# Kernel tuning notes

Measured on AMD Instinct MI355X. Metric: run time of the kernel, lower is better.

The kernel has to match this reference:

```python
import jax, jax.numpy as jnp
import numpy as np

EPS = 1e-5  # torch LayerNorm default


def _ln(x, w, b):
    m = jnp.mean(x, axis=-1, keepdims=True)
    v = jnp.mean((x - m) ** 2, axis=-1, keepdims=True)
    return (x - m) / jnp.sqrt(v + EPS) * w + b


def _conv1x1(x, w, b):
    # x: [B,C,H,W], w: [O,C], b: [O]
    return jnp.einsum('bchw,oc->bohw', x, w) + b[None, :, None, None]


def setup_inputs() -> dict:
    key = jax.random.key(0)
    ks = jax.random.split(key, 5)
    B, Cin, H, W = 8, 384, 64, 64
    D, N = 128, 512
    s = lambda k, shape, scale=0.02: jax.random.normal(k, shape, jnp.float32) * scale
    return {
        'x': jax.random.normal(ks[0], (B, Cin, H, W), jnp.float32),
        'DR': jax.random.normal(ks[1], (N, D), jnp.float32),
        'conv_in_w': s(ks[2], (D, Cin)),
        'conv_in_b': jnp.zeros((D,), jnp.float32),
        'sem_w': s(ks[3], (D, D)),
        'sem_b': jnp.zeros((D,), jnp.float32),
        'norm1_w': jnp.ones((D,), jnp.float32),
        'norm1_b': jnp.zeros((D,), jnp.float32),
        'norm2_w': jnp.ones((D,), jnp.float32),
        'norm2_b': jnp.zeros((D,), jnp.float32),
        'conv_out_w': s(ks[4], (Cin, D)),
        'conv_out_b': jnp.zeros((Cin,), jnp.float32),
    }


def reference(x, DR, conv_in_w, conv_in_b, sem_w, sem_b, norm1_w, norm1_b,
              norm2_w, norm2_b, conv_out_w, conv_out_b):
    B, _, H, W = x.shape
    N = DR.shape[0]
    x_align = _conv1x1(x, conv_in_w, conv_in_b)                      # [B,D,H,W]
    x_sem = _conv1x1(x_align, sem_w, sem_b)                          # semantic_extra (1x1 conv)
    x_sem = x_sem.transpose(0, 2, 3, 1).reshape(B, H * W, -1)        # [B,HW,D]
    x_sem = _ln(x_sem, norm1_w, norm1_b)
    dr = _ln(DR, norm2_w, norm2_b).T                                 # [D,N] (same for all batches)
    # NOTE: original applies norm_1 TWICE for the numerator (faithful quirk)
    c_u = jnp.einsum('bld,dn->bln', _ln(x_sem, norm1_w, norm1_b), dr)  # [B,HW,N]
    c_d_l = jnp.sqrt(jnp.sum(x_sem ** 2, axis=-1, keepdims=True))      # [B,HW,1]
    c_d_r = jnp.sqrt(jnp.sum(dr ** 2, axis=0, keepdims=True))[None]    # [1,1,N]
    sim = c_u / (c_d_l * c_d_r)
    sim_soft = jax.nn.softmax(sim, axis=-1)                          # [B,HW,N]
    sim2d = sim_soft.transpose(0, 2, 1).reshape(B, N, H, W)
    degrad = jnp.einsum('bln,dn->bdl', sim_soft, dr).reshape(B, -1, H, W)  # [B,D,H,W]
    # pow-mask with per-batch min-max normalization
    mask_v = jnp.max(sim2d ** 3, axis=1, keepdims=True)              # [B,1,H,W]
    mn = jnp.min(mask_v.reshape(B, -1), axis=1).reshape(B, 1, 1, 1)
    mx = jnp.max(mask_v.reshape(B, -1), axis=1).reshape(B, 1, 1, 1)
    mask_v = 1.0 - (mask_v - mn) / (mx - mn)
    # topk row selection (torch fancy indexing gives [B,B,K,N]; squeeze(1) is a no-op for B>1)
    max_values = jnp.max(sim_soft, axis=2)                           # [B,HW]
    K = (H * W) // 50
    _, top_idx = jax.lax.top_k(max_values, K)                        # [B,K]
    results = jnp.take(sim_soft, top_idx, axis=1)                    # [B,B,K,N]
    out_img = _conv1x1(degrad, conv_out_w, conv_out_b)               # [B,Cin,H,W]
    return (mask_v, out_img, results)
```

## Files before the change

### kernel.cpp

```cpp
#include <hip/hip_runtime.h>
#include <cstdint>

#define EPS 1e-5f
#define BB   8
#define CIN  384
#define HWs  4096
#define LT   32768
#define DD   128
#define NN   512
#define TOPK 81

typedef short short8 __attribute__((ext_vector_type(8)));
typedef float f32x4  __attribute__((ext_vector_type(4)));

__device__ __forceinline__ unsigned short f2bf(float x) {
  unsigned u = __float_as_uint(x);
  u += 0x7fffu + ((u >> 16) & 1u);
  return (unsigned short)(u >> 16);
}
__device__ __forceinline__ float bf2f(unsigned u16) {
  return __uint_as_float(u16 << 16);
}
__device__ __forceinline__ void put_frag(unsigned short* buf, int tile, int rc, int k, float v) {
  int ks = k >> 5, g = (k >> 3) & 3, j = k & 7;
  int basehw = ((tile * 4 + ks) * 2) * 512 + (g * 16 + rc) * 8 + j;
  unsigned short hi = f2bf(v);
  buf[basehw] = hi;
  buf[basehw + 512] = f2bf(v - bf2f(hi));
}

__global__ __launch_bounds__(64) void k_dr(const float* __restrict__ DR,
    const float* __restrict__ w2, const float* __restrict__ b2,
    const float* __restrict__ w1, const float* __restrict__ b1,
    unsigned short* __restrict__ drwF, unsigned short* __restrict__ drlnF,
    float* __restrict__ t2, float* __restrict__ rcr) {
  int n = blockIdx.x;
  int lane = threadIdx.x;
  const float* row = DR + n * DD;
  float x0 = row[lane], x1 = row[lane + 64];
  float s = x0 + x1, sq = x0 * x0 + x1 * x1;
  #pragma unroll
  for (int o = 32; o; o >>= 1) { s += __shfl_xor(s, o); sq += __shfl_xor(sq, o); }
  float m = s * (1.f / 128.f);
  float v = sq * (1.f / 128.f) - m * m;
  float inv = rsqrtf(v + EPS);
  float y0 = (x0 - m) * inv * w2[lane] + b2[lane];
  float y1 = (x1 - m) * inv * w2[lane + 64] + b2[lane + 64];
  int nt = n >> 4, cc = n & 15;
  put_frag(drwF, nt, cc, lane, y0 * w1[lane]);
  put_frag(drwF, nt, cc, lane + 64, y1 * w1[lane + 64]);
  int ks = n >> 5, gB = (n >> 3) & 3, j = n & 7;
  {
    int d = lane;
    unsigned short hi = f2bf(y0);
    int base = (((d >> 4) * 16 + ks) * 2) * 512 + (gB * 16 + (d & 15)) * 8 + j;
    drlnF[base] = hi;
    drlnF[base + 512] = f2bf(y0 - bf2f(hi));
  }
  {
    int d = lane + 64;
    unsigned short hi = f2bf(y1);
    int base = (((d >> 4) * 16 + ks) * 2) * 512 + (gB * 16 + (d & 15)) * 8 + j;
    drlnF[base] = hi;
    drlnF[base + 512] = f2bf(y1 - bf2f(hi));
  }
  float pt2 = y0 * b1[lane] + y1 * b1[lane + 64];
  float pss = y0 * y0 + y1 * y1;
  #pragma unroll
  for (int o = 32; o; o >>= 1) { pt2 += __shfl_xor(pt2, o); pss += __shfl_xor(pss, o); }
  if (lane == 0) { t2[n] = pt2; rcr[n] = rsqrtf(pss); }
}

__global__ __launch_bounds__(256) void k_bprep(const float* __restrict__ src,
                                               unsigned short* __restrict__ dst,
                                               int K) {
  int rt = blockIdx.x, kb = blockIdx.y;
  int t = threadIdx.x, m = t >> 4, kg = t & 15;
  int k0 = kb * 128 + kg * 8;
  const float* s = src + (size_t)(rt * 16 + m) * K + k0;
  float4 f0 = *(const float4*)s;
  float4 f1 = *(const float4*)(s + 4);
  float vs[8] = {f0.x, f0.y, f0.z, f0.w, f1.x, f1.y, f1.z, f1.w};
  short8 hi, lo;
  #pragma unroll
  for (int j = 0; j < 8; ++j) {
    unsigned short h = f2bf(vs[j]);
    hi[j] = (short)h;
    lo[j] = (short)f2bf(vs[j] - bf2f(h));
  }
  int nkt = K >> 5;
  int ks = k0 >> 5, g = (k0 >> 3) & 3;
  short8* D8 = (short8*)dst;
  int base = ((rt * nkt + ks) * 2) * 64 + g * 16 + m;
  D8[base] = hi;
  D8[base + 64] = lo;
}

__global__ __launch_bounds__(256, 3) void k_convsem(const float* __restrict__ x,
    const unsigned short* __restrict__ WinF, const float* __restrict__ bin,
    const unsigned short* __restrict__ semWF, const float* __restrict__ sb,
    const float* __restrict__ w1, const float* __restrict__ b1,
    unsigned short* __restrict__ ApF, float* __restrict__ rclv) {
  __shared__ float xt[CIN * 33];
  __shared__ float sredS[32][4], sredQ[32][4];
  __shared__ float rowM[32], rowI[32];
  int t = threadIdx.x;
  int w = t >> 6, lane = t & 63, m = lane & 15, g = lane >> 4;
  int l0 = blockIdx.x * 32;
  int b = l0 >> 12, hw0 = l0 & 4095;
  {
    const float* xs = x + (size_t)b * CIN * HWs + (size_t)(t >> 3) * HWs + hw0 + (t & 7) * 4;
    float4 v[12];
    #pragma unroll
    for (int r = 0; r < 12; ++r)
      v[r] = *(const float4*)(xs + (size_t)(r * 32) * HWs);
    #pragma unroll
    for (int r = 0; r < 12; ++r) {
      float* d = &xt[(r * 32 + (t >> 3)) * 33 + (t & 7) * 4];
      d[0] = v[r].x; d[1] = v[r].y; d[2] = v[r].z; d[3] = v[r].w;
    }
  }
  __syncthreads();
  const short8* B8 = (const short8*)WinF;
  f32x4 acc[2][2];
  #pragma unroll
  for (int lt = 0; lt < 2; ++lt)
    #pragma unroll
    for (int j2 = 0; j2 < 2; ++j2) acc[lt][j2] = (f32x4){0.f, 0.f, 0.f, 0.f};
  for (int ks = 0; ks < 12; ++ks) {
    short8 ah[2], al[2];
    #pragma unroll
    for (int lt = 0; lt < 2; ++lt) {
      #pragma unroll
      for (int j = 0; j < 8; ++j) {
        float xv = xt[(ks * 32 + g * 8 + j) * 33 + lt * 16 + m];
        unsigned short h = f2bf(xv);
        ah[lt][j] = (short)h;
        al[lt][j] = (short)f2bf(xv - bf2f(h));
      }
    }
    #pragma unroll
    for (int j2 = 0; j2 < 2; ++j2) {
      int dt = w * 2 + j2;
      short8 bh = B8[((dt * 12 + ks) * 2 + 0) * 64 + lane];
      short8 bl = B8[((dt * 12 + ks) * 2 + 1) * 64 + lane];
      #pragma unroll
      for (int lt = 0; lt < 2; ++lt) {
        acc[lt][j2] = __builtin_amdgcn_mfma_f32_16x16x32_bf16(ah[lt], bh, acc[lt][j2], 0, 0, 0);
        acc[lt][j2] = __builtin_amdgcn_mfma_f32_16x16x32_bf16(ah[lt], bl, acc[lt][j2], 0, 0, 0);
        acc[lt][j2] = __builtin_amdgcn_mfma_f32_16x16x32_bf16(al[lt], bh, acc[lt][j2], 0, 0, 0);
      }
    }
  }
  __syncthreads();
  unsigned int* plane = (unsigned int*)xt;
  {
    float bia[2] = {bin[w * 32 + m], bin[w * 32 + 16 + m]};
    #pragma unroll
    for (int lt = 0; lt < 2; ++lt)
      #pragma unroll
      for (int j2 = 0; j2 < 2; ++j2)
        #pragma unroll
        for (int r = 0; r < 4; ++r) {
          float v = acc[lt][j2][r] + bia[j2];
          unsigned short h = f2bf(v);
          unsigned short lo = f2bf(v - bf2f(h));
          plane[(lt * 16 + g * 4 + r) * 132 + (w * 2 + j2) * 16 + m] =
              (unsigned)h | ((unsigned)lo << 16);
        }
  }
  __syncthreads();
  const short8* S8 = (const short8*)semWF;
  f32x4 acc2[2][2];
  #pragma unroll
  for (int lt = 0; lt < 2; ++lt)
    #pragma unroll
    for (int j2 = 0; j2 < 2; ++j2) acc2[lt][j2] = (f32x4){0.f, 0.f, 0.f, 0.f};
  #pragma unroll
  for (int ks2 = 0; ks2 < 4; ++ks2) {
    short8 ah2[2], al2[2];
    #pragma unroll
    for (int lt = 0; lt < 2; ++lt) {
      const unsigned* src = &plane[(lt * 16 + m) * 132 + ks2 * 32 + g * 8];
      uint4 p0 = *(const uint4*)(src);
      uint4 p1 = *(const uint4*)(src + 4);
      unsigned uu[8] = {p0.x, p0.y, p0.z, p0.w, p1.x, p1.y, p1.z, p1.w};
      unsigned* ahp = (unsigned*)&ah2[lt];
      unsigned* alp = (unsigned*)&al2[lt];
      #pragma unroll
      for (int jj = 0; jj < 4; ++jj) {
        unsigned e0 = uu[2 * jj], e1 = uu[2 * jj + 1];
        ahp[jj] = (e0 & 0xffffu) | (e1 << 16);
        alp[jj] = (e0 >> 16) | (e1 & 0xffff0000u);
      }
    }
    #pragma unroll
    for (int j2 = 0; j2 < 2; ++j2) {
      int dt = w * 2 + j2;
      short8 bh = S8[((dt * 4 + ks2) * 2 + 0) * 64 + lane];
      short8 bl = S8[((dt * 4 + ks2) * 2 + 1) * 64 + lane];
      #pragma unroll
      for (int lt = 0; lt < 2; ++lt) {
        acc2[lt][j2] = __builtin_amdgcn_mfma_f32_16x16x32_bf16(ah2[lt], bh, acc2[lt][j2], 0, 0, 0);
        acc2[lt][j2] = __builtin_amdgcn_mfma_f32_16x16x32_bf16(ah2[lt], bl, acc2[lt][j2], 0, 0, 0);
        acc2[lt][j2] = __builtin_amdgcn_mfma_f32_16x16x32_bf16(al2[lt], bh, acc2[lt][j2], 0, 0, 0);
      }
    }
  }
  {
    float bia2[2] = {sb[w * 32 + m], sb[w * 32 + 16 + m]};
    #pragma unroll
    for (int lt = 0; lt < 2; ++lt)
      #pragma unroll
      for (int j2 = 0; j2 < 2; ++j2)
        #pragma unroll
        for (int r = 0; r < 4; ++r) acc2[lt][j2][r] += bia2[j2];
  }
  float s1[2][4], q1[2][4];
  #pragma unroll
  for (int lt = 0; lt < 2; ++lt)
    #pragma unroll
    for (int r = 0; r < 4; ++r) {
      float a = acc2[lt][0][r], b2v = acc2[lt][1][r];
      s1[lt][r] = a + b2v;
      q1[lt][r] = a * a + b2v * b2v;
    }
  #pragma unroll
  for (int o = 1; o < 16; o <<= 1)
    #pragma unroll
    for (int lt = 0; lt < 2; ++lt)
      #pragma unroll
      for (int r = 0; r < 4; ++r) {
        s1[lt][r] += __shfl_xor(s1[lt][r], o);
        q1[lt][r] += __shfl_xor(q1[lt][r], o);
      }
  if (m == 0) {
    #pragma unroll
    for (int lt = 0; lt < 2; ++lt)
      #pragma unroll
      for (int r = 0; r < 4; ++r) {
        sredS[lt * 16 + g * 4 + r][w] = s1[lt][r];
        sredQ[lt * 16 + g * 4 + r][w] = q1[lt][r];
      }
  }
  __syncthreads();
  if (t < 32) {
    float S = sredS[t][0] + sredS[t][1] + sredS[t][2] + sredS[t][3];
    float Q = sredQ[t][0] + sredQ[t][1] + sredQ[t][2] + sredQ[t][3];
    float mu = S * (1.f / 128.f);
    float var = Q * (1.f / 128.f) - mu * mu;
    rowM[t] = mu;
    rowI[t] = rsqrtf(var + EPS);
  }
  __syncthreads();
  float w1v[2] = {w1[w * 32 + m], w1[w * 32 + 16 + m]};
  float b1v[2] = {b1[w * 32 + m], b1[w * 32 + 16 + m]};
  #pragma unroll
  for (int lt = 0; lt < 2; ++lt)
    #pragma unroll
    for (int r = 0; r < 4; ++r) {
      float mu = rowM[lt * 16 + g * 4 + r];
      float iv = rowI[lt * 16 + g * 4 + r];
      float y0 = (acc2[lt][0][r] - mu) * iv * w1v[0] + b1v[0];
      float y1 = (acc2[lt][1][r] - mu) * iv * w1v[1] + b1v[1];
      acc2[lt][0][r] = y0; acc2[lt][1][r] = y1;
      s1[lt][r] = y0 + y1;
      q1[lt][r] = y0 * y0 + y1 * y1;
    }
  #pragma unroll
  for (int o = 1; o < 16; o <<= 1)
    #pragma unroll
    for (int lt = 0; lt < 2; ++lt)
      #pragma unroll
      for (int r = 0; r < 4; ++r) {
        s1[lt][r] += __shfl_xor(s1[lt][r], o);
        q1[lt][r] += __shfl_xor(q1[lt][r], o);
      }
  if (m == 0) {
    #pragma unroll
    for (int lt = 0; lt < 2; ++lt)
      #pragma unroll
      for (int r = 0; r < 4; ++r) {
        sredS[lt * 16 + g * 4 + r][w] = s1[lt][r];
        sredQ[lt * 16 + g * 4 + r][w] = q1[lt][r];
      }
  }
  __syncthreads();
  if (t < 32) {
    float S = sredS[t][0] + sredS[t][1] + sredS[t][2] + sredS[t][3];
    float Q = sredQ[t][0] + sredQ[t][1] + sredQ[t][2] + sredQ[t][3];
    float m2 = S * (1.f / 128.f);
    float v2 = Q * (1.f / 128.f) - m2 * m2;
    float inv2 = rsqrtf(v2 + EPS);
    float rcl = rsqrtf(Q);
    rowM[t] = m2;
    rowI[t] = inv2 * rcl;
    rclv[l0 + t] = rcl;
  }
  __syncthreads();
  float* planef = (float*)xt;
  #pragma unroll
  for (int lt = 0; lt < 2; ++lt)
    #pragma unroll
    for (int r = 0; r < 4; ++r) {
      float m2 = rowM[lt * 16 + g * 4 + r];
      float sc = rowI[lt * 16 + g * 4 + r];
      planef[(lt * 16 + g * 4 + r) * 132 + w * 32 + m] = (acc2[lt][0][r] - m2) * sc;
      planef[(lt * 16 + g * 4 + r) * 132 + w * 32 + 16 + m] = (acc2[lt][1][r] - m2) * sc;
    }
  __syncthreads();
  short8* O8 = (short8*)ApF;
  #pragma unroll
  for (int it = 0; it < 2; ++it) {
    int idx = it * 256 + t;
    int l = idx & 31, dq = idx >> 5;
    const float* src = &planef[l * 132 + dq * 8];
    float4 f0 = *(const float4*)src;
    float4 f1 = *(const float4*)(src + 4);
    float vs[8] = {f0.x, f0.y, f0.z, f0.w, f1.x, f1.y, f1.z, f1.w};
    short8 hi, lo;
    #pragma unroll
    for (int j = 0; j < 8; ++j) {
      unsigned short h = f2bf(vs[j]);
      hi[j] = (short)h;
      lo[j] = (short)f2bf(vs[j] - bf2f(h));
    }
    int ltg = (l0 + l) >> 4;
    int idx8 = ((ltg * 4 + (dq >> 2)) * 2) * 64 + (dq & 3) * 16 + (l & 15);
    O8[idx8] = hi;
    O8[idx8 + 64] = lo;
  }
}

__global__ __launch_bounds__(256) void k_scores(const unsigned short* __restrict__ ApF,
    const unsigned short* __restrict__ drwF, const float* __restrict__ t2g,
    const float* __restrict__ rcrg, const float* __restrict__ rclg,
    unsigned short* __restrict__ pF, float* __restrict__ maxv) {
  __shared__ __align__(16) float sredM[32][4];
  __shared__ __align__(16) float sredS[32][4];
  __shared__ __align__(16) unsigned short plds[32 * 520];
  int t = threadIdx.x;
  int w = t >> 6, lane = t & 63, c = lane & 15, g = lane >> 4;
  int l0 = blockIdx.x * 32;
  int lt0 = blockIdx.x * 2;
  const short8* A8 = (const short8*)ApF;
  const short8* B8 = (const short8*)drwF;
  f32x4 acc[2][8];
  #pragma unroll
  for (int il = 0; il < 2; ++il)
    #pragma unroll
    for (int jn = 0; jn < 8; ++jn) acc[il][jn] = (f32x4){0.f, 0.f, 0.f, 0.f};
  #pragma unroll
  for (int ks = 0; ks < 4; ++ks) {
    short8 ah0 = A8[((lt0 * 4 + ks) * 2 + 0) * 64 + lane];
    short8 al0 = A8[((lt0 * 4 + ks) * 2 + 1) * 64 + lane];
    short8 ah1 = A8[(((lt0 + 1) * 4 + ks) * 2 + 0) * 64 + lane];
    short8 al1 = A8[(((lt0 + 1) * 4 + ks) * 2 + 1) * 64 + lane];
    #pragma unroll
    for (int jn = 0; jn < 8; ++jn) {
      int nt = w * 8 + jn;
      short8 bh = B8[((nt * 4 + ks) * 2 + 0) * 64 + lane];
      short8 bl = B8[((nt * 4 + ks) * 2 + 1) * 64 + lane];
      acc[0][jn] = __builtin_amdgcn_mfma_f32_16x16x32_bf16(ah0, bh, acc[0][jn], 0, 0, 0);
      acc[0][jn] = __builtin_amdgcn_mfma_f32_16x16x32_bf16(ah0, bl, acc[0][jn], 0, 0, 0);
      acc[0][jn] = __builtin_amdgcn_mfma_f32_16x16x32_bf16(al0, bh, acc[0][jn], 0, 0, 0);
      acc[1][jn] = __builtin_amdgcn_mfma_f32_16x16x32_bf16(ah1, bh, acc[1][jn], 0, 0, 0);
      acc[1][jn] = __builtin_amdgcn_mfma_f32_16x16x32_bf16(ah1, bl, acc[1][jn], 0, 0, 0);
      acc[1][jn] = __builtin_amdgcn_mfma_f32_16x16x32_bf16(al1, bh, acc[1][jn], 0, 0, 0);
    }
  }
  float rcrv[8], t2v[8];
  #pragma unroll
  for (int jn = 0; jn < 8; ++jn) {
    int n = w * 128 + jn * 16 + c;
    rcrv[jn] = rcrg[n]; t2v[jn] = t2g[n];
  }
  float rclr[2][4];
  #pragma unroll
  for (int il = 0; il < 2; ++il)
    #pragma unroll
    for (int r = 0; r < 4; ++r)
      rclr[il][r] = rclg[l0 + il * 16 + g * 4 + r];
  float M[2][4];
  #pragma unroll
  for (int il = 0; il < 2; ++il)
    #pragma unroll
    for (int r = 0; r < 4; ++r) M[il][r] = -1e30f;
  #pragma unroll
  for (int il = 0; il < 2; ++il)
    #pragma unroll
    for (int jn = 0; jn < 8; ++jn) {
      f32x4 a = acc[il][jn];
      #pragma unroll
      for (int r = 0; r < 4; ++r) {
        float s = rcrv[jn] * (a[r] + rclr[il][r] * t2v[jn]);
        a[r] = s;
        M[il][r] = fmaxf(M[il][r], s);
      }
      acc[il][jn] = a;
    }
  #pragma unroll
  for (int o = 1; o < 16; o <<= 1)
    #pragma unroll
    for (int il = 0; il < 2; ++il)
      #pragma unroll
      for (int r = 0; r < 4; ++r)
        M[il][r] = fmaxf(M[il][r], __shfl_xor(M[il][r], o));
  if (c == 0) {
    #pragma unroll
    for (int il = 0; il < 2; ++il)
      #pragma unroll
      for (int r = 0; r < 4; ++r)
        sredM[il * 16 + g * 4 + r][w] = M[il][r];
  }
  __syncthreads();
  float Mf[2][4];
  #pragma unroll
  for (int il = 0; il < 2; ++il)
    #pragma unroll
    for (int r = 0; r < 4; ++r) {
      f32x4 mv = *(const f32x4*)(&sredM[il * 16 + g * 4 + r][0]);
      Mf[il][r] = fmaxf(fmaxf(mv[0], mv[1]), fmaxf(mv[2], mv[3]));
    }
  float S[2][4];
  #pragma unroll
  for (int il = 0; il < 2; ++il)
    #pragma unroll
    for (int r = 0; r < 4; ++r) S[il][r] = 0.f;
  #pragma unroll
  for (int il = 0; il < 2; ++il)
    #pragma unroll
    for (int jn = 0; jn < 8; ++jn) {
      f32x4 a = acc[il][jn];
      #pragma unroll
      for (int r = 0; r < 4; ++r) {
        float e = __expf(a[r] - Mf[il][r]);
        a[r] = e;
        S[il][r] += e;
      }
      acc[il][jn] = a;
    }
  #pragma unroll
  for (int o = 1; o < 16; o <<= 1)
    #pragma unroll
    for (int il = 0; il < 2; ++il)
      #pragma unroll
      for (int r = 0; r < 4; ++r)
        S[il][r] += __shfl_xor(S[il][r], o);
  if (c == 0) {
    #pragma unroll
    for (int il = 0; il < 2; ++il)
      #pragma unroll
      for (int r = 0; r < 4; ++r)
        sredS[il * 16 + g * 4 + r][w] = S[il][r];
  }
  __syncthreads();
  float RS[2][4];
  #pragma unroll
  for (int il = 0; il < 2; ++il)
    #pragma unroll
    for (int r = 0; r < 4; ++r) {
      f32x4 sv = *(const f32x4*)(&sredS[il * 16 + g * 4 + r][0]);
      float tot = sv[0] + sv[1] + sv[2] + sv[3];
      RS[il][r] = 1.f / tot;
    }
  if (w == 0 && c == 0) {
    #pragma unroll
    for (int il = 0; il < 2; ++il)
      #pragma unroll
      for (int r = 0; r < 4; ++r)
        maxv[l0 + il * 16 + g * 4 + r] = RS[il][r];
  }
  #pragma unroll
  for (int il = 0; il < 2; ++il)
    #pragma unroll
    for (int jn = 0; jn < 8; ++jn)
      #pragma unroll
      for (int r = 0; r < 4; ++r)
        plds[(il * 16 + g * 4 + r) * 520 + w * 128 + jn * 16 + c] =
            f2bf(acc[il][jn][r] * RS[il][r]);
  __syncthreads();
  short8* P8o = (short8*)pF;
  #pragma unroll
  for (int it = 0; it < 8; ++it) {
    int slot = it * 256 + t;
    int ltl = slot >> 10;
    int ks = (slot >> 6) & 15;
    int gB = (slot >> 4) & 3;
    int mrow = slot & 15;
    int row = ltl * 16 + mrow;
    int n0 = ks * 32 + gB * 8;
    short8 v = *(const short8*)(&plds[row * 520 + n0]);
    P8o[blockIdx.x * 2048 + slot] = v;
  }
}

__global__ __launch_bounds__(256) void k_deg(const unsigned short* __restrict__ pF,
    const unsigned short* __restrict__ drlnF, const unsigned short* __restrict__ WoF,
    const float* __restrict__ bo, float* __restrict__ out_img) {
  __shared__ float smem[64 * 132];
  int t = threadIdx.x;
  int w = t >> 6, lane = t & 63, c = lane & 15, g = lane >> 4;
  int l0 = blockIdx.x * 64;
  int lt0 = l0 >> 4;
  const short8* P8 = (const short8*)pF;
  const short8* D8 = (const short8*)drlnF;
  const short8* W8 = (const short8*)WoF;
  f32x4 acc[4][2];
  #pragma unroll
  for (int lt = 0; lt < 4; ++lt)
    #pragma unroll
    for (int j2 = 0; j2 < 2; ++j2) acc[lt][j2] = (f32x4){0.f, 0.f, 0.f, 0.f};
  for (int ks = 0; ks < 16; ++ks) {
    short8 a0 = P8[((lt0 + 0) * 16 + ks) * 64 + lane];
    short8 a1 = P8[((lt0 + 1) * 16 + ks) * 64 + lane];
    short8 a2 = P8[((lt0 + 2) * 16 + ks) * 64 + lane];
    short8 a3 = P8[((lt0 + 3) * 16 + ks) * 64 + lane];
    #pragma unroll
    for (int j2 = 0; j2 < 2; ++j2) {
      int dt = w * 2 + j2;
      short8 bh = D8[((dt * 16 + ks) * 2 + 0) * 64 + lane];
      short8 bl = D8[((dt * 16 + ks) * 2 + 1) * 64 + lane];
      acc[0][j2] = __builtin_amdgcn_mfma_f32_16x16x32_bf16(a0, bh, acc[0][j2], 0, 0, 0);
      acc[0][j2] = __builtin_amdgcn_mfma_f32_16x16x32_bf16(a0, bl, acc[0][j2], 0, 0, 0);
      acc[1][j2] = __builtin_amdgcn_mfma_f32_16x16x32_bf16(a1, bh, acc[1][j2], 0, 0, 0);
      acc[1][j2] = __builtin_amdgcn_mfma_f32_16x16x32_bf16(a1, bl, acc[1][j2], 0, 0, 0);
      acc[2][j2] = __builtin_amdgcn_mfma_f32_16x16x32_bf16(a2, bh, acc[2][j2], 0, 0, 0);
      acc[2][j2] = __builtin_amdgcn_mfma_f32_16x16x32_bf16(a2, bl, acc[2][j2], 0, 0, 0);
      acc[3][j2] = __builtin_amdgcn_mfma_f32_16x16x32_bf16(a3, bh, acc[3][j2], 0, 0, 0);
      acc[3][j2] = __builtin_amdgcn_mfma_f32_16x16x32_bf16(a3, bl, acc[3][j2], 0, 0, 0);
    }
  }
  #pragma unroll
  for (int lt = 0; lt < 4; ++lt)
    #pragma unroll
    for (int j2 = 0; j2 < 2; ++j2)
      #pragma unroll
      for (int r = 0; r < 4; ++r)
        smem[(lt * 16 + g * 4 + r) * 132 + w * 32 + j2 * 16 + c] = acc[lt][j2][r];
  __syncthreads();
  f32x4 acc2[4][6];
  #pragma unroll
  for (int lt = 0; lt < 4; ++lt)
    #pragma unroll
    for (int ot = 0; ot < 6; ++ot) acc2[lt][ot] = (f32x4){0.f, 0.f, 0.f, 0.f};
  #pragma unroll
  for (int ks2 = 0; ks2 < 4; ++ks2) {
    short8 dh[4];
    #pragma unroll
    for (int lt = 0; lt < 4; ++lt) {
      const float* src = &smem[(lt * 16 + c) * 132 + ks2 * 32 + g * 8];
      float4 f0 = *(const float4*)src;
      float4 f1 = *(const float4*)(src + 4);
      float vs[8] = {f0.x, f0.y, f0.z, f0.w, f1.x, f1.y, f1.z, f1.w};
      #pragma unroll
      for (int j = 0; j < 8; ++j) dh[lt][j] = (short)f2bf(vs[j]);
    }
    #pragma unroll
    for (int ot = 0; ot < 6; ++ot) {
      int otg = w * 6 + ot;
      short8 wh = W8[((otg * 4 + ks2) * 2 + 0) * 64 + lane];
      short8 wl = W8[((otg * 4 + ks2) * 2 + 1) * 64 + lane];
      #pragma unroll
      for (int lt = 0; lt < 4; ++lt) {
        acc2[lt][ot] = __builtin_amdgcn_mfma_f32_16x16x32_bf16(dh[lt], wh, acc2[lt][ot], 0, 0, 0);
        acc2[lt][ot] = __builtin_amdgcn_mfma_f32_16x16x32_bf16(dh[lt], wl, acc2[lt][ot], 0, 0, 0);
      }
    }
  }
  __syncthreads();
  int b = l0 >> 12, hw0 = l0 & 4095;
  float* ob = out_img + (size_t)b * CIN * HWs + hw0;
  float bov[6];
  #pragma unroll
  for (int ot = 0; ot < 6; ++ot) bov[ot] = bo[w * 96 + ot * 16 + c];
  for (int ot = 0; ot < 6; ++ot) {
    #pragma unroll
    for (int lt = 0; lt < 4; ++lt)
      #pragma unroll
      for (int r = 0; r < 4; ++r)
        smem[(lt * 16 + g * 4 + r) * 65 + w * 16 + c] = acc2[lt][ot][r] + bov[ot];
    __syncthreads();
    #pragma unroll
    for (int i = 0; i < 16; ++i) {
      int idx = t + i * 256;
      int o_l = idx >> 6, ll = idx & 63;
      int o = (o_l >> 4) * 96 + ot * 16 + (o_l & 15);
      ob[(size_t)o * HWs + ll] = smem[ll * 65 + o_l];
    }
    __syncthreads();
  }
}

__global__ __launch_bounds__(256) void k_mask(const float* __restrict__ maxv,
                                              float* __restrict__ outm) {
  int b = blockIdx.x, t = threadIdx.x;
  float c[16];
  float mn = 1e30f, mx = -1e30f;
  #pragma unroll
  for (int j = 0; j < 16; ++j) {
    float x = maxv[b * HWs + t + j * 256];
    float cc = x * x * x;
    c[j] = cc;
    mn = fminf(mn, cc); mx = fmaxf(mx, cc);
  }
  #pragma unroll
  for (int o = 32; o; o >>= 1) { mn = fminf(mn, __shfl_xor(mn, o)); mx = fmaxf(mx, __shfl_xor(mx, o)); }
  __shared__ float smn[4], smx[4];
  int w = t >> 6;
  if ((t & 63) == 0) { smn[w] = mn; smx[w] = mx; }
  __syncthreads();
  mn = fminf(fminf(smn[0], smn[1]), fminf(smn[2], smn[3]));
  mx = fmaxf(fmaxf(smx[0], smx[1]), fmaxf(smx[2], smx[3]));
  float sc = 1.f / (mx - mn);
  #pragma unroll
  for (int j = 0; j < 16; ++j)
    outm[b * HWs + t + j * 256] = 1.f - (c[j] - mn) * sc;
}

__global__ __launch_bounds__(256) void k_topk(const float* __restrict__ maxv,
                                              int* __restrict__ tix) {
  __shared__ unsigned int hist[4][256];
  __shared__ unsigned long long slist[TOPK];
  __shared__ unsigned long long bc_prefix;
  __shared__ int bc_need, scount;
  int b = blockIdx.x, t = threadIdx.x;
  int w = t >> 6;
  unsigned long long key[16];
  #pragma unroll
  for (int j = 0; j < 16; ++j) {
    int idx = t + j * 256;
    unsigned int bits = __float_as_uint(maxv[b * HWs + idx]);
    key[j] = ((unsigned long long)bits << 12) | (unsigned)(4095 - idx);
  }
  if (t == 0) { bc_prefix = 0ull; bc_need = TOPK; scount = 0; }
  for (int r = 0; r < 6; ++r) {
    int shift = 40 - 8 * r;
    unsigned int* hflat = (unsigned int*)hist;
    hflat[t] = 0; hflat[t + 256] = 0; hflat[t + 512] = 0; hflat[t + 768] = 0;
    __syncthreads();
    unsigned long long prefix = bc_prefix;
    int bins[16];
    #pragma unroll
    for (int j = 0; j < 16; ++j)
      bins[j] = ((key[j] >> (shift + 8)) == prefix) ? (int)((key[j] >> shift) & 255) : -1;
    #pragma unroll
    for (int j = 0; j < 16; ++j) {
      if (bins[j] >= 0) {
        int cnt = 1;
        #pragma unroll
        for (int j2 = j + 1; j2 < 16; ++j2)
          if (bins[j2] == bins[j]) { bins[j2] = -1; ++cnt; }
        atomicAdd(&hist[w][bins[j]], (unsigned)cnt);
      }
    }
    __syncthreads();
    if (t < 64) {
      int cb[4], s = 0;
      #pragma unroll
      for (int j = 0; j < 4; ++j) {
        int bin = 255 - (t * 4 + j);
        cb[j] = (int)(hist[0][bin] + hist[1][bin] + hist[2][bin] + hist[3][bin]);
        s += cb[j];
      }
      int P = s;
      #pragma unroll
      for (int o = 1; o < 64; o <<= 1) {
        int u = __shfl_up(P, o);
        if (t >= o) P += u;
      }
      int need = bc_need;
      unsigned long long mask = __ballot(P >= need);
      int first = __ffsll((long long)mask) - 1;
      if (t == first) {
        int acc = P - s;
        #pragma unroll
        for (int j = 0; j < 4; ++j) {
          if (acc + cb[j] >= need) {
            bc_prefix = (prefix << 8) | (unsigned)(255 - (t * 4 + j));
            bc_need = need - acc;
            break;
          }
          acc += cb[j];
        }
      }
    }
    __syncthreads();
  }
  unsigned long long K81 = bc_prefix;
  #pragma unroll
  for (int j = 0; j < 16; ++j)
    if (key[j] >= K81) {
      int pos = atomicAdd(&scount, 1);
      slist[pos] = key[j];
    }
  __syncthreads();
  if (t < TOPK) {
    unsigned long long mine = slist[t];
    int rank = 0;
    for (int i = 0; i < TOPK; ++i) rank += (slist[i] > mine) ? 1 : 0;
    tix[b * TOPK + rank] = 4095 - (int)(mine & 0xFFFull);
  }
}

__global__ __launch_bounds__(128) void k_gather(const unsigned short* __restrict__ pF,
    const int* __restrict__ tix, float* __restrict__ outr) {
  int gB_ = blockIdx.x;
  int k = gB_ % TOPK;
  int bb = gB_ / TOPK;
  int b2 = bb & 7, b = bb >> 3;
  int l = b * HWs + tix[b2 * TOPK + k];
  int lt = l >> 4, mrow = l & 15;
  int t = threadIdx.x;
  int ks = t >> 3, gq = (t >> 1) & 3, j0 = (t & 1) * 4;
  int base = ((lt * 16 + ks) * 64 + gq * 16 + mrow) * 8 + j0;
  const unsigned* src = (const unsigned*)(pF + base);
  unsigned u0 = src[0], u1 = src[1];
  float4 v = {bf2f(u0 & 0xffffu), bf2f(u0 >> 16), bf2f(u1 & 0xffffu), bf2f(u1 >> 16)};
  *(float4*)(outr + (size_t)gB_ * NN + t * 4) = v;
}

extern "C" void kernel_launch(void* const* d_in, const int* in_sizes, int n_in,
                              void* d_out, int out_size, void* d_ws, size_t ws_size,
                              hipStream_t stream) {
  const float* x    = (const float*)d_in[0];
  const float* DR   = (const float*)d_in[1];
  const float* win  = (const float*)d_in[2];
  const float* bin  = (const float*)d_in[3];
  const float* sw   = (const float*)d_in[4];
  const float* sb   = (const float*)d_in[5];
  const float* n1w  = (const float*)d_in[6];
  const float* n1b  = (const float*)d_in[7];
  const float* n2w  = (const float*)d_in[8];
  const float* n2b  = (const float*)d_in[9];
  const float* wout = (const float*)d_in[10];
  const float* bout = (const float*)d_in[11];
  float* out = (float*)d_out;
  float* W = (float*)d_ws;

  unsigned short* drwF  = (unsigned short*)(W);
  float* t2   = W + 65536;
  float* rcr  = W + 66048;
  float* rclv = W + 66560;
  float* maxv = W + 99328;
  unsigned short* drlnF = (unsigned short*)(W + 132096);
  unsigned short* WoF   = (unsigned short*)(W + 197632);
  unsigned short* WinF  = (unsigned short*)(W + 246784);
  unsigned short* semWF = (unsigned short*)(W + 295936);
  unsigned short* ApF   = (unsigned short*)(W + 312320);
  unsigned short* pF    = (unsigned short*)(W + 4506624);
  int*   tix  = (int*)(W + 12895232);

  float* out_mask = out;
  float* out_img  = out + 32768;
  float* out_res  = out + 32768 + 12582912;

  k_dr     <<<NN, 64, 0, stream>>>(DR, n2w, n2b, n1w, n1b, drwF, drlnF, t2, rcr);
  k_bprep  <<<dim3(8, 3),  256, 0, stream>>>(win,  WinF,  CIN);
  k_bprep  <<<dim3(8, 1),  256, 0, stream>>>(sw,   semWF, DD);
  k_bprep  <<<dim3(24, 1), 256, 0, stream>>>(wout, WoF,   DD);
  k_convsem<<<1024, 256, 0, stream>>>(x, WinF, bin, semWF, sb, n1w, n1b, ApF, rclv);
  k_scores <<<1024, 256, 0, stream>>>(ApF, drwF, t2, rcr, rclv, pF, maxv);
  k_deg    <<<512,  256, 0, stream>>>(pF, drlnF, WoF, bout, out_img);
  k_mask   <<<BB,   256, 0, stream>>>(maxv, out_mask);
  k_topk   <<<BB,   256, 0, stream>>>(maxv, tix);
  k_gather <<<BB * BB * TOPK, 128, 0, stream>>>(pF, tix, out_res);
}
```

Before: 227.4 us.

## Fuse degradation and output conv into scores kernel; merge mask into topk

The degradation GEMM (softmax probabilities times normalized DR) and the output 1x1 conv now run inside the scores kernel, reading the bf16 probabilities straight from LDS instead of re-reading them from global memory in a separate kernel. The output image is written directly from registers as float4 stores, with no LDS transpose. The LDS row stride is changed to 528, and the mask min-max kernel is merged into the top-k kernel, so two launches and one global pass over the probabilities are removed. The trade-off is more registers and LDS per block (launch bounds now ask for 4 blocks), smaller 32-row tiles that reuse the DR and weight fragments less, and strided output writes.

Result: faster. 217.5 us (-4.4%).

```diff
diff --git a/kernel.cpp b/kernel.cpp
--- a/kernel.cpp
+++ b/kernel.cpp
@@ -9,6 +9,7 @@
 #define DD   128
 #define NN   512
 #define TOPK 81
+#define PSTR 528
 
 typedef short short8 __attribute__((ext_vector_type(8)));
 typedef float f32x4  __attribute__((ext_vector_type(4)));
@@ -332,13 +333,16 @@
   }
 }
 
-__global__ __launch_bounds__(256) void k_scores(const unsigned short* __restrict__ ApF,
+__global__ __launch_bounds__(256, 4) void k_sdeg(const unsigned short* __restrict__ ApF,
     const unsigned short* __restrict__ drwF, const float* __restrict__ t2g,
     const float* __restrict__ rcrg, const float* __restrict__ rclg,
-    unsigned short* __restrict__ pF, float* __restrict__ maxv) {
+    const unsigned short* __restrict__ drlnF, const unsigned short* __restrict__ WoF,
+    const float* __restrict__ bo,
+    unsigned short* __restrict__ pF, float* __restrict__ maxv,
+    float* __restrict__ out_img) {
   __shared__ __align__(16) float sredM[32][4];
   __shared__ __align__(16) float sredS[32][4];
-  __shared__ __align__(16) unsigned short plds[32 * 520];
+  __shared__ __align__(16) unsigned short plds[32 * PSTR];
   int t = threadIdx.x;
   int w = t >> 6, lane = t & 63, c = lane & 15, g = lane >> 4;
   int l0 = blockIdx.x * 32;
@@ -477,9 +481,30 @@
     for (int jn = 0; jn < 8; ++jn)
       #pragma unroll
       for (int r = 0; r < 4; ++r)
-        plds[(il * 16 + g * 4 + r) * 520 + w * 128 + jn * 16 + c] =
+        plds[(il * 16 + g * 4 + r) * PSTR + w * 128 + jn * 16 + c] =
             f2bf(acc[il][jn][r] * RS[il][r]);
   __syncthreads();
+  const short8* D8 = (const short8*)drlnF;
+  f32x4 accd[2][2];
+  #pragma unroll
+  for (int lt = 0; lt < 2; ++lt)
+    #pragma unroll
+    for (int j2 = 0; j2 < 2; ++j2) accd[lt][j2] = (f32x4){0.f, 0.f, 0.f, 0.f};
+  for (int ks = 0; ks < 16; ++ks) {
+    const unsigned short* sp = &plds[c * PSTR + ks * 32 + g * 8];
+    short8 pa0 = *(const short8*)sp;
+    short8 pa1 = *(const short8*)(sp + 16 * PSTR);
+    #pragma unroll
+    for (int j2 = 0; j2 < 2; ++j2) {
+      int dt = w * 2 + j2;
+      short8 bh = D8[((dt * 16 + ks) * 2 + 0) * 64 + lane];
+      short8 bl = D8[((dt * 16 + ks) * 2 + 1) * 64 + lane];
+      accd[0][j2] = __builtin_amdgcn_mfma_f32_16x16x32_bf16(pa0, bh, accd[0][j2], 0, 0, 0);
+      accd[0][j2] = __builtin_amdgcn_mfma_f32_16x16x32_bf16(pa0, bl, accd[0][j2], 0, 0, 0);
+      accd[1][j2] = __builtin_amdgcn_mfma_f32_16x16x32_bf16(pa1, bh, accd[1][j2], 0, 0, 0);
+      accd[1][j2] = __builtin_amdgcn_mfma_f32_16x16x32_bf16(pa1, bl, accd[1][j2], 0, 0, 0);
+    }
+  }
   short8* P8o = (short8*)pF;
   #pragma unroll
   for (int it = 0; it < 8; ++it) {
@@ -490,66 +515,31 @@
     int mrow = slot & 15;
     int row = ltl * 16 + mrow;
     int n0 = ks * 32 + gB * 8;
-    short8 v = *(const short8*)(&plds[row * 520 + n0]);
+    short8 v = *(const short8*)(&plds[row * PSTR + n0]);
     P8o[blockIdx.x * 2048 + slot] = v;
   }
-}
-
-__global__ __launch_bounds__(256) void k_deg(const unsigned short* __restrict__ pF,
-    const unsigned short* __restrict__ drlnF, const unsigned short* __restrict__ WoF,
-    const float* __restrict__ bo, float* __restrict__ out_img) {
-  __shared__ float smem[64 * 132];
-  int t = threadIdx.x;
-  int w = t >> 6, lane = t & 63, c = lane & 15, g = lane >> 4;
-  int l0 = blockIdx.x * 64;
-  int lt0 = l0 >> 4;
-  const short8* P8 = (const short8*)pF;
-  const short8* D8 = (const short8*)drlnF;
+  __syncthreads();
+  float* smem2 = (float*)plds;
+  #pragma unroll
+  for (int lt = 0; lt < 2; ++lt)
+    #pragma unroll
+    for (int j2 = 0; j2 < 2; ++j2)
+      #pragma unroll
+      for (int r = 0; r < 4; ++r)
+        smem2[(lt * 16 + g * 4 + r) * 132 + w * 32 + j2 * 16 + c] = accd[lt][j2][r];
+  __syncthreads();
   const short8* W8 = (const short8*)WoF;
-  f32x4 acc[4][2];
-  #pragma unroll
-  for (int lt = 0; lt < 4; ++lt)
-    #pragma unroll
-    for (int j2 = 0; j2 < 2; ++j2) acc[lt][j2] = (f32x4){0.f, 0.f, 0.f, 0.f};
-  for (int ks = 0; ks < 16; ++ks) {
-    short8 a0 = P8[((lt0 + 0) * 16 + ks) * 64 + lane];
-    short8 a1 = P8[((lt0 + 1) * 16 + ks) * 64 + lane];
-    short8 a2 = P8[((lt0 + 2) * 16 + ks) * 64 + lane];
-    short8 a3 = P8[((lt0 + 3) * 16 + ks) * 64 + lane];
-    #pragma unroll
-    for (int j2 = 0; j2 < 2; ++j2) {
-      int dt = w * 2 + j2;
-      short8 bh = D8[((dt * 16 + ks) * 2 + 0) * 64 + lane];
-      short8 bl = D8[((dt * 16 + ks) * 2 + 1) * 64 + lane];
-      acc[0][j2] = __builtin_amdgcn_mfma_f32_16x16x32_bf16(a0, bh, acc[0][j2], 0, 0, 0);
-      acc[0][j2] = __builtin_amdgcn_mfma_f32_16x16x32_bf16(a0, bl, acc[0][j2], 0, 0, 0);
-      acc[1][j2] = __builtin_amdgcn_mfma_f32_16x16x32_bf16(a1, bh, acc[1][j2], 0, 0, 0);
-      acc[1][j2] = __builtin_amdgcn_mfma_f32_16x16x32_bf16(a1, bl, acc[1][j2], 0, 0, 0);
-      acc[2][j2] = __builtin_amdgcn_mfma_f32_16x16x32_bf16(a2, bh, acc[2][j2], 0, 0, 0);
-      acc[2][j2] = __builtin_amdgcn_mfma_f32_16x16x32_bf16(a2, bl, acc[2][j2], 0, 0, 0);
-      acc[3][j2] = __builtin_amdgcn_mfma_f32_16x16x32_bf16(a3, bh, acc[3][j2], 0, 0, 0);
-      acc[3][j2] = __builtin_amdgcn_mfma_f32_16x16x32_bf16(a3, bl, acc[3][j2], 0, 0, 0);
-    }
-  }
-  #pragma unroll
-  for (int lt = 0; lt < 4; ++lt)
-    #pragma unroll
-    for (int j2 = 0; j2 < 2; ++j2)
-      #pragma unroll
-      for (int r = 0; r < 4; ++r)
-        smem[(lt * 16 + g * 4 + r) * 132 + w * 32 + j2 * 16 + c] = acc[lt][j2][r];
-  __syncthreads();
-  f32x4 acc2[4][6];
-  #pragma unroll
-  for (int lt = 0; lt < 4; ++lt)
-    #pragma unroll
-    for (int ot = 0; ot < 6; ++ot) acc2[lt][ot] = (f32x4){0.f, 0.f, 0.f, 0.f};
+  f32x4 acco[2][6];
+  #pragma unroll
+  for (int lt = 0; lt < 2; ++lt)
+    #pragma unroll
+    for (int ot = 0; ot < 6; ++ot) acco[lt][ot] = (f32x4){0.f, 0.f, 0.f, 0.f};
   #pragma unroll
   for (int ks2 = 0; ks2 < 4; ++ks2) {
-    short8 dh[4];
-    #pragma unroll
-    for (int lt = 0; lt < 4; ++lt) {
-      const float* src = &smem[(lt * 16 + c) * 132 + ks2 * 32 + g * 8];
+    short8 dh[2];
+    #pragma unroll
+    for (int lt = 0; lt < 2; ++lt) {
+      const float* src = &smem2[(lt * 16 + c) * 132 + ks2 * 32 + g * 8];
       float4 f0 = *(const float4*)src;
       float4 f1 = *(const float4*)(src + 4);
       float vs[8] = {f0.x, f0.y, f0.z, f0.w, f1.x, f1.y, f1.z, f1.w};
@@ -562,68 +552,34 @@
       short8 wh = W8[((otg * 4 + ks2) * 2 + 0) * 64 + lane];
       short8 wl = W8[((otg * 4 + ks2) * 2 + 1) * 64 + lane];
       #pragma unroll
-      for (int lt = 0; lt < 4; ++lt) {
-        acc2[lt][ot] = __builtin_amdgcn_mfma_f32_16x16x32_bf16(dh[lt], wh, acc2[lt][ot], 0, 0, 0);
-        acc2[lt][ot] = __builtin_amdgcn_mfma_f32_16x16x32_bf16(dh[lt], wl, acc2[lt][ot], 0, 0, 0);
-      }
-    }
-  }
-  __syncthreads();
+      for (int lt = 0; lt < 2; ++lt) {
+        acco[lt][ot] = __builtin_amdgcn_mfma_f32_16x16x32_bf16(dh[lt], wh, acco[lt][ot], 0, 0, 0);
+        acco[lt][ot] = __builtin_amdgcn_mfma_f32_16x16x32_bf16(dh[lt], wl, acco[lt][ot], 0, 0, 0);
+      }
+    }
+  }
   int b = l0 >> 12, hw0 = l0 & 4095;
   float* ob = out_img + (size_t)b * CIN * HWs + hw0;
-  float bov[6];
-  #pragma unroll
-  for (int ot = 0; ot < 6; ++ot) bov[ot] = bo[w * 96 + ot * 16 + c];
+  #pragma unroll
   for (int ot = 0; ot < 6; ++ot) {
-    #pragma unroll
-    for (int lt = 0; lt < 4; ++lt)
-      #pragma unroll
-      for (int r = 0; r < 4; ++r)
-        smem[(lt * 16 + g * 4 + r) * 65 + w * 16 + c] = acc2[lt][ot][r] + bov[ot];
-    __syncthreads();
-    #pragma unroll
-    for (int i = 0; i < 16; ++i) {
-      int idx = t + i * 256;
-      int o_l = idx >> 6, ll = idx & 63;
-      int o = (o_l >> 4) * 96 + ot * 16 + (o_l & 15);
-      ob[(size_t)o * HWs + ll] = smem[ll * 65 + o_l];
-    }
-    __syncthreads();
-  }
-}
-
-__global__ __launch_bounds__(256) void k_mask(const float* __restrict__ maxv,
+    float bov = bo[w * 96 + ot * 16 + c];
+    #pragma unroll
+    for (int lt = 0; lt < 2; ++lt) {
+      f32x4 vv = acco[lt][ot];
+      float4 o4 = {vv[0] + bov, vv[1] + bov, vv[2] + bov, vv[3] + bov};
+      *(float4*)(ob + (size_t)(w * 96 + ot * 16 + c) * HWs + lt * 16 + g * 4) = o4;
+    }
+  }
+}
+
+__global__ __launch_bounds__(256) void k_topk(const float* __restrict__ maxv,
+                                              int* __restrict__ tix,
                                               float* __restrict__ outm) {
-  int b = blockIdx.x, t = threadIdx.x;
-  float c[16];
-  float mn = 1e30f, mx = -1e30f;
-  #pragma unroll
-  for (int j = 0; j < 16; ++j) {
-    float x = maxv[b * HWs + t + j * 256];
-    float cc = x * x * x;
-    c[j] = cc;
-    mn = fminf(mn, cc); mx = fmaxf(mx, cc);
-  }
-  #pragma unroll
-  for (int o = 32; o; o >>= 1) { mn = fminf(mn, __shfl_xor(mn, o)); mx = fmaxf(mx, __shfl_xor(mx, o)); }
-  __shared__ float smn[4], smx[4];
-  int w = t >> 6;
-  if ((t & 63) == 0) { smn[w] = mn; smx[w] = mx; }
-  __syncthreads();
-  mn = fminf(fminf(smn[0], smn[1]), fminf(smn[2], smn[3]));
-  mx = fmaxf(fmaxf(smx[0], smx[1]), fmaxf(smx[2], smx[3]));
-  float sc = 1.f / (mx - mn);
-  #pragma unroll
-  for (int j = 0; j < 16; ++j)
-    outm[b * HWs + t + j * 256] = 1.f - (c[j] - mn) * sc;
-}
-
-__global__ __launch_bounds__(256) void k_topk(const float* __restrict__ maxv,
-                                              int* __restrict__ tix) {
   __shared__ unsigned int hist[4][256];
   __shared__ unsigned long long slist[TOPK];
   __shared__ unsigned long long bc_prefix;
   __shared__ int bc_need, scount;
+  __shared__ float smn[4], smx[4];
   int b = blockIdx.x, t = threadIdx.x;
   int w = t >> 6;
   unsigned long long key[16];
@@ -632,6 +588,27 @@
     int idx = t + j * 256;
     unsigned int bits = __float_as_uint(maxv[b * HWs + idx]);
     key[j] = ((unsigned long long)bits << 12) | (unsigned)(4095 - idx);
+  }
+  {
+    float c3[16];
+    float mn = 1e30f, mx = -1e30f;
+    #pragma unroll
+    for (int j = 0; j < 16; ++j) {
+      float x = __uint_as_float((unsigned)(key[j] >> 12));
+      float cc = x * x * x;
+      c3[j] = cc;
+      mn = fminf(mn, cc); mx = fmaxf(mx, cc);
+    }
+    #pragma unroll
+    for (int o = 32; o; o >>= 1) { mn = fminf(mn, __shfl_xor(mn, o)); mx = fmaxf(mx, __shfl_xor(mx, o)); }
+    if ((t & 63) == 0) { smn[w] = mn; smx[w] = mx; }
+    __syncthreads();
+    mn = fminf(fminf(smn[0], smn[1]), fminf(smn[2], smn[3]));
+    mx = fmaxf(fmaxf(smx[0], smx[1]), fmaxf(smx[2], smx[3]));
+    float sc = 1.f / (mx - mn);
+    #pragma unroll
+    for (int j = 0; j < 16; ++j)
+      outm[b * HWs + t + j * 256] = 1.f - (c3[j] - mn) * sc;
   }
   if (t == 0) { bc_prefix = 0ull; bc_need = TOPK; scount = 0; }
   for (int r = 0; r < 6; ++r) {
@@ -760,9 +737,8 @@
   k_bprep  <<<dim3(8, 1),  256, 0, stream>>>(sw,   semWF, DD);
   k_bprep  <<<dim3(24, 1), 256, 0, stream>>>(wout, WoF,   DD);
   k_convsem<<<1024, 256, 0, stream>>>(x, WinF, bin, semWF, sb, n1w, n1b, ApF, rclv);
-  k_scores <<<1024, 256, 0, stream>>>(ApF, drwF, t2, rcr, rclv, pF, maxv);
-  k_deg    <<<512,  256, 0, stream>>>(pF, drlnF, WoF, bout, out_img);
-  k_mask   <<<BB,   256, 0, stream>>>(maxv, out_mask);
-  k_topk   <<<BB,   256, 0, stream>>>(maxv, tix);
+  k_sdeg   <<<1024, 256, 0, stream>>>(ApF, drwF, t2, rcr, rclv, drlnF, WoF, bout,
+                                      pF, maxv, out_img);
+  k_topk   <<<BB,   256, 0, stream>>>(maxv, tix, out_mask);
   k_gather <<<BB * BB * TOPK, 128, 0, stream>>>(pF, tix, out_res);
 }
```
